# Kernel optimization log

Measured on AMD Instinct MI355X. Metric: run time of the kernel, lower is better.

## Reference

```python
import jax, jax.numpy as jnp
import numpy as np

N_NODES = 100000
N_EDGES = 1600000
N_GRAPHS = 512
NUM_REL = 3


def setup_inputs() -> dict:
    key = jax.random.key(0)
    ks = jax.random.split(key, 16)
    shape_idx = jax.random.randint(ks[0], (N_NODES,), 0, 16)
    color_idx = jax.random.randint(ks[1], (N_NODES,), 0, 8)
    node_feats = jnp.stack([shape_idx, color_idx], axis=1)  # [N,2] int
    edge_index = jax.random.randint(ks[2], (2, N_EDGES), 0, N_NODES)
    edge_type = jax.random.randint(ks[3], (N_EDGES,), 0, NUM_REL)
    batch = jnp.sort(jax.random.randint(ks[4], (N_NODES,), 0, N_GRAPHS))
    s = lambda k, sh: jax.random.normal(k, sh, dtype=jnp.float32) * 0.05
    return {
        'node_feats': node_feats,
        'edge_index': edge_index,
        'edge_type': edge_type,
        'batch': batch,
        'shape_emb': s(ks[5], (16, 8)),
        'color_emb': s(ks[6], (8, 8)),
        'pre_w': s(ks[7], (16, 32)),
        'pre_b': jnp.zeros((32,), jnp.float32),
        'root1': s(ks[8], (32, 64)),
        'rel1': s(ks[9], (NUM_REL, 32, 64)),
        'bias1': jnp.zeros((64,), jnp.float32),
        'root2': s(ks[10], (64, 64)),
        'rel2': s(ks[11], (NUM_REL, 64, 64)),
        'bias2': jnp.zeros((64,), jnp.float32),
        'cls_w': s(ks[12], (64, 10)),
        'cls_b': jnp.zeros((10,), jnp.float32),
    }


def rgcn_conv(x, edge_index, edge_type, root, rel_w, bias):
    # PyG RGCNConv: out_i = x_i @ root + sum_r mean_{j in N_r(i)} x_j @ W_r + bias
    src, dst = edge_index[0], edge_index[1]
    out = x @ root + bias
    xs = x[src]  # [E, in] gathered source features
    for r in range(NUM_REL):
        m = (edge_type == r).astype(x.dtype)  # [E]
        msg = (xs @ rel_w[r]) * m[:, None]  # [E, out]
        agg = jax.ops.segment_sum(msg, dst, num_segments=N_NODES)
        cnt = jax.ops.segment_sum(m, dst, num_segments=N_NODES)
        out = out + agg / jnp.maximum(cnt, 1.0)[:, None]
    return out


def reference(node_feats, edge_index, edge_type, batch, shape_emb, color_emb,
              pre_w, pre_b, root1, rel1, bias1, root2, rel2, bias2, cls_w, cls_b):
    x = jnp.concatenate([shape_emb[node_feats[:, 0]], color_emb[node_feats[:, 1]]], axis=1)  # [N,16]
    x = jax.nn.relu(x @ pre_w + pre_b)  # [N,32]
    x = jax.nn.relu(rgcn_conv(x, edge_index, edge_type, root1, rel1, bias1))  # [N,64]
    x = jax.nn.relu(rgcn_conv(x, edge_index, edge_type, root2, rel2, bias2))  # [N,64]
    # global_mean_pool over graph ids
    s = jax.ops.segment_sum(x, batch, num_segments=N_GRAPHS)
    c = jax.ops.segment_sum(jnp.ones((x.shape[0],), x.dtype), batch, num_segments=N_GRAPHS)
    pooled = s / jnp.maximum(c, 1.0)[:, None]  # [G,64]
    return pooled @ cls_w + cls_b  # [G,num_classes]
```

## Files before the change

kernel.cpp:

```cpp
#include <hip/hip_runtime.h>

#define NN 100000
#define NE 1600000
#define NG 512

#define BSH 9
#define NB 196
#define EPB 8192
#define NAB ((NE + EPB - 1) / EPB)
#define CAP 9216

__global__ __launch_bounds__(256) void k_embed(
    const int* __restrict__ nf, const float* __restrict__ semb,
    const float* __restrict__ cemb, const float* __restrict__ pw,
    const float* __restrict__ pb, float* __restrict__ x1)
{
  int gid = blockIdx.x * 256 + threadIdx.x;
  bool valid = gid < NN;
  int i = valid ? gid : NN - 1;
  int sf = nf[2 * i], cf = nf[2 * i + 1];
  float x0[16];
#pragma unroll
  for (int k = 0; k < 8; ++k) x0[k] = semb[sf * 8 + k];
#pragma unroll
  for (int k = 0; k < 8; ++k) x0[8 + k] = cemb[cf * 8 + k];
  float acc[32];
#pragma unroll
  for (int j = 0; j < 32; ++j) acc[j] = pb[j];
#pragma unroll
  for (int k = 0; k < 16; ++k) {
    float xv = x0[k];
#pragma unroll
    for (int j = 0; j < 32; ++j) acc[j] += xv * pw[k * 32 + j];
  }
  if (valid) {
    float4* o = (float4*)(x1 + (size_t)i * 32);
#pragma unroll
    for (int j4 = 0; j4 < 8; ++j4) {
      float4 v;
      v.x = fmaxf(acc[4 * j4 + 0], 0.f);
      v.y = fmaxf(acc[4 * j4 + 1], 0.f);
      v.z = fmaxf(acc[4 * j4 + 2], 0.f);
      v.w = fmaxf(acc[4 * j4 + 3], 0.f);
      o[j4] = v;
    }
  }
}


__global__ __launch_bounds__(256) void kA_count(
    const int* __restrict__ ei, int* __restrict__ bkt_cnt)
{
  __shared__ int lh[NB];
  for (int b = threadIdx.x; b < NB; b += 256) lh[b] = 0;
  __syncthreads();
  int base = blockIdx.x * EPB;
#pragma unroll
  for (int i = 0; i < EPB / 256; ++i) {
    int e = base + i * 256 + threadIdx.x;
    if (e < NE) atomicAdd(&lh[ei[NE + e] >> BSH], 1);
  }
  __syncthreads();
  for (int b = threadIdx.x; b < NB; b += 256)
    if (lh[b]) atomicAdd(&bkt_cnt[b], lh[b]);
}

__global__ __launch_bounds__(256) void kA_scan(
    const int* __restrict__ bkt_cnt, int* __restrict__ bkt_base,
    int* __restrict__ bkt_cur)
{
  __shared__ int sm[2][256];
  int t = threadIdx.x;
  int v = (t < NB) ? bkt_cnt[t] : 0;
  sm[0][t] = v;
  __syncthreads();
  int cur = 0;
#pragma unroll
  for (int off = 1; off < 256; off <<= 1) {
    int add = (t >= off) ? sm[cur][t - off] : 0;
    sm[cur ^ 1][t] = sm[cur][t] + add;
    __syncthreads();
    cur ^= 1;
  }
  if (t < NB) {
    int ex = sm[cur][t] - v;
    bkt_base[t] = ex;
    bkt_cur[t] = ex;
  }
  if (t == 0) bkt_base[NB] = NE;
}

__global__ __launch_bounds__(256) void kA_scatter(
    const int* __restrict__ ei, const int* __restrict__ et,
    int* __restrict__ bkt_cur, int* __restrict__ binned)
{
  __shared__ int packA[EPB];
  __shared__ unsigned char bktA[EPB];
  __shared__ int lh[NB], grun[NB], lcur[NB];
  for (int b = threadIdx.x; b < NB; b += 256) { lh[b] = 0; lcur[b] = 0; }
  __syncthreads();
  int base = blockIdx.x * EPB;
#pragma unroll
  for (int i = 0; i < EPB / 256; ++i) {
    int p = i * 256 + threadIdx.x;
    int e = base + p;
    if (e < NE) {
      int src = ei[e], dst = ei[NE + e], ty = et[e];
      int b = dst >> BSH;
      packA[p] = src | (ty << 17) | ((dst & 511) << 19);
      bktA[p] = (unsigned char)b;
      atomicAdd(&lh[b], 1);
    } else {
      bktA[p] = 255;
    }
  }
  __syncthreads();
  for (int b = threadIdx.x; b < NB; b += 256)
    grun[b] = lh[b] ? atomicAdd(&bkt_cur[b], lh[b]) : 0;
  __syncthreads();
#pragma unroll
  for (int i = 0; i < EPB / 256; ++i) {
    int p = i * 256 + threadIdx.x;
    int b = bktA[p];
    if (b != 255) {
      int off = atomicAdd(&lcur[b], 1);
      binned[grun[b] + off] = packA[p];
    }
  }
}

__global__ __launch_bounds__(512) void kB_build(
    const int* __restrict__ bkt_base, const int* __restrict__ binned,
    int* __restrict__ rs3, int* __restrict__ ep)
{
  __shared__ int stage[CAP];
  __shared__ int ldeg3[1536], lrs3[1536], lcur3[1536];
  __shared__ int sm[2][512];
  int b = blockIdx.x;
  int t = threadIdx.x;
  int p0 = bkt_base[b], p1 = bkt_base[b + 1];
  int cnt = p1 - p0;
  int nodes0 = b << BSH;
  int nnodes = NN - nodes0 < 512 ? NN - nodes0 : 512;
  ldeg3[t] = 0; ldeg3[t + 512] = 0; ldeg3[t + 1024] = 0;
  lcur3[t] = 0; lcur3[t + 512] = 0; lcur3[t + 1024] = 0;
  __syncthreads();
  for (int p = t; p < cnt; p += 512) {
    int pk = binned[p0 + p];
    if (p < CAP) stage[p] = pk;
    int key = ((pk >> 19) & 511) * 3 + ((pk >> 17) & 3);
    atomicAdd(&ldeg3[key], 1);
  }
  __syncthreads();
  int s0 = ldeg3[3 * t], s1 = ldeg3[3 * t + 1], s2 = ldeg3[3 * t + 2];
  int tot = s0 + s1 + s2;
  sm[0][t] = tot;
  __syncthreads();
  int cur = 0;
#pragma unroll
  for (int off = 1; off < 512; off <<= 1) {
    int add = (t >= off) ? sm[cur][t - off] : 0;
    sm[cur ^ 1][t] = sm[cur][t] + add;
    __syncthreads();
    cur ^= 1;
  }
  int ex = sm[cur][t] - tot;
  int r0 = p0 + ex, r1 = r0 + s0, r2 = r1 + s1;
  lrs3[3 * t] = r0;
  lrs3[3 * t + 1] = r1;
  lrs3[3 * t + 2] = r2;
  if (t < nnodes) {
    size_t base3 = (size_t)(nodes0 + t) * 3;
    rs3[base3 + 0] = r0;
    rs3[base3 + 1] = r1;
    rs3[base3 + 2] = r2;
  }
  if (b == NB - 1 && t == 0) rs3[(size_t)NN * 3] = NE;
  __syncthreads();
  for (int p = t; p < cnt; p += 512) {
    int pk = (p < CAP) ? stage[p] : binned[p0 + p];
    int key = ((pk >> 19) & 511) * 3 + ((pk >> 17) & 3);
    int off = atomicAdd(&lcur3[key], 1);
    ep[lrs3[key] + off] = pk & 0x1FFFF;
  }
}

template <int IN>
__global__ __launch_bounds__(256) void k_agg(
    const float* __restrict__ x, const int* __restrict__ rs3,
    const int* __restrict__ ep, float* __restrict__ h)
{
  constexpr int LPE = IN / 4;
  constexpr int DPW = (IN == 32) ? 2 : 1;
  constexpr int SW = 64 / DPW;
  constexpr int EPI = SW / LPE;
  int tid = threadIdx.x;
  int wid = (blockIdx.x * 256 + tid) >> 6;
  int lane = tid & 63;
  int sub = lane / SW;
  int sl = lane % SW;
  int k4 = sl % LPE;
  int es = sl / LPE;
  int d = wid * DPW + sub;
  if (d >= NN) return;
  int q0 = rs3[3 * d + 0];
  int q1 = rs3[3 * d + 1];
  int q2 = rs3[3 * d + 2];
  int q3 = rs3[3 * d + 3];
  float4 a0 = make_float4(0.f, 0.f, 0.f, 0.f);
  float4 a1 = make_float4(0.f, 0.f, 0.f, 0.f);
  float4 a2 = make_float4(0.f, 0.f, 0.f, 0.f);
#pragma unroll 2
  for (int p = q0; p < q3; p += EPI) {
    int idx = p + es;
    bool val = idx < q3;
    int e = ep[val ? idx : q3 - 1];
    float4 v = *(const float4*)(x + (size_t)e * IN + k4 * 4);
    float m0 = (val && idx < q1) ? 1.f : 0.f;
    float m1 = (val && idx >= q1 && idx < q2) ? 1.f : 0.f;
    float m2 = (val && idx >= q2) ? 1.f : 0.f;
    a0.x = fmaf(m0, v.x, a0.x); a0.y = fmaf(m0, v.y, a0.y);
    a0.z = fmaf(m0, v.z, a0.z); a0.w = fmaf(m0, v.w, a0.w);
    a1.x = fmaf(m1, v.x, a1.x); a1.y = fmaf(m1, v.y, a1.y);
    a1.z = fmaf(m1, v.z, a1.z); a1.w = fmaf(m1, v.w, a1.w);
    a2.x = fmaf(m2, v.x, a2.x); a2.y = fmaf(m2, v.y, a2.y);
    a2.z = fmaf(m2, v.z, a2.z); a2.w = fmaf(m2, v.w, a2.w);
  }
#pragma unroll
  for (int off = LPE; off < SW; off <<= 1) {
    a0.x += __shfl_xor(a0.x, off, 64); a0.y += __shfl_xor(a0.y, off, 64);
    a0.z += __shfl_xor(a0.z, off, 64); a0.w += __shfl_xor(a0.w, off, 64);
    a1.x += __shfl_xor(a1.x, off, 64); a1.y += __shfl_xor(a1.y, off, 64);
    a1.z += __shfl_xor(a1.z, off, 64); a1.w += __shfl_xor(a1.w, off, 64);
    a2.x += __shfl_xor(a2.x, off, 64); a2.y += __shfl_xor(a2.y, off, 64);
    a2.z += __shfl_xor(a2.z, off, 64); a2.w += __shfl_xor(a2.w, off, 64);
  }
  if (es == 0) {
    float* hd = h + (size_t)d * 3 * IN;
    float c0 = (float)(q1 - q0 > 0 ? q1 - q0 : 1);
    float c1 = (float)(q2 - q1 > 0 ? q2 - q1 : 1);
    float c2 = (float)(q3 - q2 > 0 ? q3 - q2 : 1);
    float4 o;
    o.x = a0.x / c0; o.y = a0.y / c0; o.z = a0.z / c0; o.w = a0.w / c0;
    *(float4*)(hd + 0 * IN + k4 * 4) = o;
    o.x = a1.x / c1; o.y = a1.y / c1; o.z = a1.z / c1; o.w = a1.w / c1;
    *(float4*)(hd + 1 * IN + k4 * 4) = o;
    o.x = a2.x / c2; o.y = a2.y / c2; o.z = a2.z / c2; o.w = a2.w / c2;
    *(float4*)(hd + 2 * IN + k4 * 4) = o;
  }
}

template <int IN>
__global__ __launch_bounds__(512) void k_mat(
    const float* __restrict__ x, const float* __restrict__ h,
    const float* __restrict__ root, const float* __restrict__ rel,
    const float* __restrict__ bias, float* __restrict__ y)
{
  __shared__ float smem[3 * IN][65];
  const int tid = threadIdx.x;
  const int node0 = blockIdx.x * 64;
  const int n = tid & 63;
  const int j0 = __builtin_amdgcn_readfirstlane((tid >> 6) * 8);

  constexpr int F4 = IN / 4;
  constexpr int NPF = (64 * F4) / 512;

  for (int idx = tid; idx < 64 * F4; idx += 512) {
    int nn = idx / F4, c4 = idx % F4;
    int node = node0 + nn;
    float4 v = make_float4(0.f, 0.f, 0.f, 0.f);
    if (node < NN) v = *(const float4*)(x + (size_t)node * IN + c4 * 4);
    smem[c4 * 4 + 0][nn] = v.x;
    smem[c4 * 4 + 1][nn] = v.y;
    smem[c4 * 4 + 2][nn] = v.z;
    smem[c4 * 4 + 3][nn] = v.w;
  }
#pragma unroll
  for (int r = 0; r < 2; ++r) {
    for (int idx = tid; idx < 64 * F4; idx += 512) {
      int nn = idx / F4, c4 = idx % F4;
      int node = node0 + nn;
      float4 v = make_float4(0.f, 0.f, 0.f, 0.f);
      if (node < NN) v = *(const float4*)(h + ((size_t)node * 3 + r) * IN + c4 * 4);
      smem[(1 + r) * IN + c4 * 4 + 0][nn] = v.x;
      smem[(1 + r) * IN + c4 * 4 + 1][nn] = v.y;
      smem[(1 + r) * IN + c4 * 4 + 2][nn] = v.z;
      smem[(1 + r) * IN + c4 * 4 + 3][nn] = v.w;
    }
  }
  __syncthreads();

  float4 pf[NPF];
#pragma unroll
  for (int u = 0; u < NPF; ++u) {
    int idx = u * 512 + tid;
    int nn = idx / F4, c4 = idx % F4;
    int node = node0 + nn;
    pf[u] = make_float4(0.f, 0.f, 0.f, 0.f);
    if (node < NN) pf[u] = *(const float4*)(h + ((size_t)node * 3 + 2) * IN + c4 * 4);
  }

  float acc[8];
#pragma unroll
  for (int j = 0; j < 8; ++j) acc[j] = bias[j0 + j];

  auto mm = [&](const float* __restrict__ W, int row0) {
#pragma unroll 4
    for (int k = 0; k < IN; ++k) {
      float sk = smem[row0 + k][n];
      const float* w = W + (size_t)k * 64 + j0;
#pragma unroll
      for (int j = 0; j < 8; ++j) acc[j] = fmaf(sk, w[j], acc[j]);
    }
  };

  mm(root, 0);
  mm(rel, IN);
  mm(rel + (size_t)IN * 64, 2 * IN);
  __syncthreads();

#pragma unroll
  for (int u = 0; u < NPF; ++u) {
    int idx = u * 512 + tid;
    int nn = idx / F4, c4 = idx % F4;
    smem[c4 * 4 + 0][nn] = pf[u].x;
    smem[c4 * 4 + 1][nn] = pf[u].y;
    smem[c4 * 4 + 2][nn] = pf[u].z;
    smem[c4 * 4 + 3][nn] = pf[u].w;
  }
  __syncthreads();
  mm(rel + (size_t)2 * IN * 64, 0);

  int node = node0 + n;
  if (node < NN) {
    float4* o = (float4*)(y + (size_t)node * 64 + j0);
    float4 v;
    v.x = fmaxf(acc[0], 0.f);
    v.y = fmaxf(acc[1], 0.f);
    v.z = fmaxf(acc[2], 0.f);
    v.w = fmaxf(acc[3], 0.f);
    o[0] = v;
    v.x = fmaxf(acc[4], 0.f);
    v.y = fmaxf(acc[5], 0.f);
    v.z = fmaxf(acc[6], 0.f);
    v.w = fmaxf(acc[7], 0.f);
    o[1] = v;
  }
}

__global__ __launch_bounds__(256) void k_pool(
    const float* __restrict__ x3, const int* __restrict__ batch,
    float* __restrict__ pooled, float* __restrict__ gcnt)
{
  int gwave = (blockIdx.x * 256 + threadIdx.x) >> 6;
  int lane = threadIdx.x & 63;
  int n0 = gwave * 64;
  if (n0 >= NN) return;
  int n1 = n0 + 64 < NN ? n0 + 64 : NN;
  int gcur = batch[n0];
  float acc = 0.f;
  int run = 0;
  for (int n = n0; n < n1; ++n) {
    int g = batch[n];
    if (g != gcur) {
      atomicAdd(&pooled[gcur * 64 + lane], acc);
      if (lane == 0) atomicAdd(&gcnt[gcur], (float)run);
      acc = 0.f; run = 0; gcur = g;
    }
    acc += x3[(size_t)n * 64 + lane];
    ++run;
  }
  atomicAdd(&pooled[gcur * 64 + lane], acc);
  if (lane == 0) atomicAdd(&gcnt[gcur], (float)run);
}

__global__ __launch_bounds__(256) void k_cls(
    const float* __restrict__ pooled, const float* __restrict__ gcnt,
    const float* __restrict__ cw, const float* __restrict__ cb, float* __restrict__ out)
{
  int t = blockIdx.x * 256 + threadIdx.x;
  if (t >= NG * 10) return;
  int g = t / 10, c = t % 10;
  float cf = fmaxf(gcnt[g], 1.f);
  float acc = cb[c];
#pragma unroll 8
  for (int k = 0; k < 64; ++k)
    acc += (pooled[g * 64 + k] / cf) * cw[k * 10 + c];
  out[t] = acc;
}

extern "C" void kernel_launch(void* const* d_in, const int* in_sizes, int n_in,
                              void* d_out, int out_size, void* d_ws, size_t ws_size,
                              hipStream_t stream)
{
  const int* nf = (const int*)d_in[0];
  const int* ei = (const int*)d_in[1];
  const int* et = (const int*)d_in[2];
  const int* batch = (const int*)d_in[3];
  const float* semb = (const float*)d_in[4];
  const float* cemb = (const float*)d_in[5];
  const float* pw = (const float*)d_in[6];
  const float* pb = (const float*)d_in[7];
  const float* root1 = (const float*)d_in[8];
  const float* rel1 = (const float*)d_in[9];
  const float* bias1 = (const float*)d_in[10];
  const float* root2 = (const float*)d_in[11];
  const float* rel2 = (const float*)d_in[12];
  const float* bias2 = (const float*)d_in[13];
  const float* cw = (const float*)d_in[14];
  const float* cb = (const float*)d_in[15];
  float* out = (float*)d_out;

  char* ws = (char*)d_ws;
  size_t off = 0;
  auto alloc = [&](size_t bytes) {
    char* p = ws + off;
    off += (bytes + 255) & ~(size_t)255;
    return p;
  };
  int* bkt_cnt = (int*)alloc((size_t)NB * 4);
  int* bkt_base = (int*)alloc((size_t)(NB + 1) * 4);
  int* bkt_cur = (int*)alloc((size_t)NB * 4);
  int* rs3 = (int*)alloc(((size_t)NN * 3 + 1) * 4);
  int* ep = (int*)alloc((size_t)NE * 4 + 256);
  float* xA = (float*)alloc((size_t)NN * 64 * 4);
  float* xB = (float*)alloc((size_t)NN * 64 * 4);
  float* h = (float*)alloc((size_t)3 * NN * 64 * 4);
  float* pooled = (float*)alloc((size_t)NG * 64 * 4);
  float* gcnt = (float*)alloc((size_t)NG * 4);
  int* binned = (int*)h;
  (void)ws_size; (void)in_sizes; (void)n_in; (void)out_size;

  hipMemsetAsync(bkt_cnt, 0, (size_t)NB * 4, stream);
  k_embed<<<(NN + 255) / 256, 256, 0, stream>>>(nf, semb, cemb, pw, pb, xB);

  kA_count<<<NAB, 256, 0, stream>>>(ei, bkt_cnt);
  kA_scan<<<1, 256, 0, stream>>>(bkt_cnt, bkt_base, bkt_cur);
  kA_scatter<<<NAB, 256, 0, stream>>>(ei, et, bkt_cur, binned);
  kB_build<<<NB, 512, 0, stream>>>(bkt_base, binned, rs3, ep);

  int matgrid = (NN + 63) / 64;

  k_agg<32><<<(NN / 2 + 3) / 4 + 1, 256, 0, stream>>>(xB, rs3, ep, h);
  k_mat<32><<<matgrid, 512, 0, stream>>>(xB, h, root1, rel1, bias1, xA);
  k_agg<64><<<(NN + 3) / 4, 256, 0, stream>>>(xA, rs3, ep, h);
  k_mat<64><<<matgrid, 512, 0, stream>>>(xA, h, root2, rel2, bias2, xB);

  hipMemsetAsync(pooled, 0, (size_t)NG * 64 * 4, stream);
  hipMemsetAsync(gcnt, 0, (size_t)NG * 4, stream);
  int nwaves = (NN + 63) / 64;
  k_pool<<<(nwaves + 3) / 4, 256, 0, stream>>>(xB, batch, pooled, gcnt);
  k_cls<<<(NG * 10 + 255) / 256, 256, 0, stream>>>(pooled, gcnt, cw, cb, out);
}
```

Measured before the change: 307.9 us.

## Double-buffer k_mat input tiles to overlap global loads with matmul

Rewrites the k_mat staging so each of the four input tiles (x and three relation aggregates) is loaded into registers while the previous tile's matmul runs. Two shared-memory buffers alternate between tiles. Before, three tiles were loaded up front and only the last was prefetched. This cuts shared memory from 3*IN to 2*IN rows, which may allow more blocks per CU. The cost is extra barriers per stage and added register pressure.

After: 294.3 us. 1.05x faster.

```diff
diff --git a/kernel.cpp b/kernel.cpp
--- a/kernel.cpp
+++ b/kernel.cpp
@@ -256,94 +256,89 @@
     const float* __restrict__ root, const float* __restrict__ rel,
     const float* __restrict__ bias, float* __restrict__ y)
 {
-  __shared__ float smem[3 * IN][65];
+  constexpr int F4 = IN / 4;
+  constexpr int NPF = (64 * F4) / 512;
+  __shared__ float B[2][IN][65];
+
   const int tid = threadIdx.x;
   const int node0 = blockIdx.x * 64;
   const int n = tid & 63;
   const int j0 = __builtin_amdgcn_readfirstlane((tid >> 6) * 8);
 
-  constexpr int F4 = IN / 4;
-  constexpr int NPF = (64 * F4) / 512;
-
-  for (int idx = tid; idx < 64 * F4; idx += 512) {
-    int nn = idx / F4, c4 = idx % F4;
-    int node = node0 + nn;
-    float4 v = make_float4(0.f, 0.f, 0.f, 0.f);
-    if (node < NN) v = *(const float4*)(x + (size_t)node * IN + c4 * 4);
-    smem[c4 * 4 + 0][nn] = v.x;
-    smem[c4 * 4 + 1][nn] = v.y;
-    smem[c4 * 4 + 2][nn] = v.z;
-    smem[c4 * 4 + 3][nn] = v.w;
-  }
-#pragma unroll
-  for (int r = 0; r < 2; ++r) {
-    for (int idx = tid; idx < 64 * F4; idx += 512) {
-      int nn = idx / F4, c4 = idx % F4;
-      int node = node0 + nn;
-      float4 v = make_float4(0.f, 0.f, 0.f, 0.f);
-      if (node < NN) v = *(const float4*)(h + ((size_t)node * 3 + r) * IN + c4 * 4);
-      smem[(1 + r) * IN + c4 * 4 + 0][nn] = v.x;
-      smem[(1 + r) * IN + c4 * 4 + 1][nn] = v.y;
-      smem[(1 + r) * IN + c4 * 4 + 2][nn] = v.z;
-      smem[(1 + r) * IN + c4 * 4 + 3][nn] = v.w;
-    }
-  }
-  __syncthreads();
-
-  float4 pf[NPF];
+  float4 p[NPF];
+  int s_nn[NPF], s_c4[NPF];
 #pragma unroll
   for (int u = 0; u < NPF; ++u) {
     int idx = u * 512 + tid;
-    int nn = idx / F4, c4 = idx % F4;
-    int node = node0 + nn;
-    pf[u] = make_float4(0.f, 0.f, 0.f, 0.f);
-    if (node < NN) pf[u] = *(const float4*)(h + ((size_t)node * 3 + 2) * IN + c4 * 4);
-  }
+    s_nn[u] = idx / F4;
+    s_c4[u] = idx % F4;
+  }
+
+  auto issue = [&](int s) {
+#pragma unroll
+    for (int u = 0; u < NPF; ++u) {
+      int node = node0 + s_nn[u];
+      float4 v = make_float4(0.f, 0.f, 0.f, 0.f);
+      if (node < NN) {
+        const float* src = (s == 0) ? x + (size_t)node * IN
+                                    : h + ((size_t)node * 3 + (s - 1)) * IN;
+        v = *(const float4*)(src + s_c4[u] * 4);
+      }
+      p[u] = v;
+    }
+  };
+
+  auto commit = [&](int buf) {
+#pragma unroll
+    for (int u = 0; u < NPF; ++u) {
+      int r0 = s_c4[u] * 4, nn = s_nn[u];
+      B[buf][r0 + 0][nn] = p[u].x;
+      B[buf][r0 + 1][nn] = p[u].y;
+      B[buf][r0 + 2][nn] = p[u].z;
+      B[buf][r0 + 3][nn] = p[u].w;
+    }
+  };
 
   float acc[8];
 #pragma unroll
   for (int j = 0; j < 8; ++j) acc[j] = bias[j0 + j];
 
-  auto mm = [&](const float* __restrict__ W, int row0) {
+  auto mm = [&](const float* __restrict__ W, int buf) {
 #pragma unroll 4
     for (int k = 0; k < IN; ++k) {
-      float sk = smem[row0 + k][n];
+      float sk = B[buf][k][n];
       const float* w = W + (size_t)k * 64 + j0;
 #pragma unroll
       for (int j = 0; j < 8; ++j) acc[j] = fmaf(sk, w[j], acc[j]);
     }
   };
 
-  mm(root, 0);
-  mm(rel, IN);
-  mm(rel + (size_t)IN * 64, 2 * IN);
-  __syncthreads();
-
-#pragma unroll
-  for (int u = 0; u < NPF; ++u) {
-    int idx = u * 512 + tid;
-    int nn = idx / F4, c4 = idx % F4;
-    smem[c4 * 4 + 0][nn] = pf[u].x;
-    smem[c4 * 4 + 1][nn] = pf[u].y;
-    smem[c4 * 4 + 2][nn] = pf[u].z;
-    smem[c4 * 4 + 3][nn] = pf[u].w;
-  }
-  __syncthreads();
-  mm(rel + (size_t)2 * IN * 64, 0);
+  issue(0);
+  commit(0);
+  __syncthreads();
+
+  const float* W[4] = {root, rel, rel + (size_t)IN * 64,
+                       rel + (size_t)2 * IN * 64};
+#pragma unroll
+  for (int s = 0; s < 4; ++s) {
+    if (s < 3) issue(s + 1);
+    mm(W[s], s & 1);
+    if (s < 3) {
+      __syncthreads();
+      commit((s + 1) & 1);
+      __syncthreads();
+    }
+  }
 
   int node = node0 + n;
   if (node < NN) {
     float4* o = (float4*)(y + (size_t)node * 64 + j0);
     float4 v;
-    v.x = fmaxf(acc[0], 0.f);
-    v.y = fmaxf(acc[1], 0.f);
-    v.z = fmaxf(acc[2], 0.f);
-    v.w = fmaxf(acc[3], 0.f);
+    v.x = fmaxf(acc[0], 0.f); v.y = fmaxf(acc[1], 0.f);
+    v.z = fmaxf(acc[2], 0.f); v.w = fmaxf(acc[3], 0.f);
     o[0] = v;
-    v.x = fmaxf(acc[4], 0.f);
-    v.y = fmaxf(acc[5], 0.f);
-    v.z = fmaxf(acc[6], 0.f);
-    v.w = fmaxf(acc[7], 0.f);
+    v.x = fmaxf(acc[4], 0.f); v.y = fmaxf(acc[5], 0.f);
+    v.z = fmaxf(acc[6], 0.f); v.w = fmaxf(acc[7], 0.f);
     o[1] = v;
   }
 }
```
